# Kernel optimization log

Measured on AMD Instinct MI355X. Metric: run time of the kernel, lower is better.

Reference implementation:

```python
import math
import jax, jax.numpy as jnp
import numpy as np

B, T, C = 2, 768, 64
N_HEAD = 64
HEAD_DIM = C // N_HEAD  # = 1 (forced by the Kronecker-lift shape constraint)


def _alibi_slopes(n_heads):
    def pow2_slopes(n):
        start = 2 ** (-2 ** (-(math.log2(n) - 3)))
        return [start * (start ** i) for i in range(n)]
    if math.log2(n_heads).is_integer():
        s = pow2_slopes(n_heads)
    else:
        closest = 2 ** math.floor(math.log2(n_heads))
        s = pow2_slopes(closest)
        s.extend(pow2_slopes(2 * closest)[0::2][: n_heads - closest])
    return np.asarray(s, dtype=np.float32)


def _kron_block_apply(z, tmp):
    """Apply M.T where M = block_diag_h(kron(eye(hd), tmp[h])). z:(B,T,C), tmp:(H,hd,hd).
    Per head-block, for z reshaped (a,d) over (hd,hd): out[a,c] = sum_d tmp[h,c,d] * z[a,d]."""
    Bz, Tz, Cz = z.shape
    H, hd, _ = tmp.shape
    zr = z.reshape(Bz, Tz, H, hd, hd)
    return jnp.einsum('bthad,hcd->bthac', zr, tmp).reshape(Bz, Tz, Cz)


def setup_inputs() -> dict:
    key = jax.random.key(0)
    kx, kw, kv, kp = jax.random.split(key, 4)
    x = jax.random.normal(kx, (B, T, C), dtype=jnp.float32)
    W_attn = jax.random.normal(kw, (2 * C, C), dtype=jnp.float32) * 0.02
    v_tmp = jax.random.normal(kv, (N_HEAD, HEAD_DIM, HEAD_DIM), dtype=jnp.float32)
    proj_tmp = jax.random.normal(kp, (N_HEAD, HEAD_DIM, HEAD_DIM), dtype=jnp.float32)
    return {"x": x, "W_attn": W_attn, "v_tmp": v_tmp, "proj_tmp": proj_tmp}


def reference(x, W_attn, v_tmp, proj_tmp):
    Bx, Tx, Cx = x.shape
    H = v_tmp.shape[0]
    head_dim = Cx // H
    # q, k projection (use_v=True -> c_attn maps C -> 2C, no bias)
    qk = x @ W_attn.T
    q, k = jnp.split(qk, 2, axis=-1)
    # Kronecker-lifted V transform (block-diagonal structure applied directly)
    v = _kron_block_apply(x, v_tmp)
    # (B,T,H,d) -> (B,H,T,d)
    q = q.reshape(Bx, Tx, H, head_dim).transpose(0, 2, 1, 3)
    k = k.reshape(Bx, Tx, H, head_dim).transpose(0, 2, 1, 3)
    v = v.reshape(Bx, Tx, H, head_dim).transpose(0, 2, 1, 3)
    scale = 1.0 / math.sqrt(head_dim)
    scores = jnp.einsum('bhid,bhjd->bhij', q, k) * scale
    # ALiBi bias: positions clamped at 0 (NOTE: source has no causal -inf mask)
    pos = jnp.minimum(jnp.arange(Tx)[None, :] - jnp.arange(Tx)[:, None], 0).astype(x.dtype)
    slopes = jnp.asarray(_alibi_slopes(H), dtype=x.dtype)
    scores = scores + slopes[None, :, None, None] * pos[None, None, :, :]
    w = jax.nn.softmax(scores, axis=-1)
    y = jnp.einsum('bhij,bhjd->bhid', w, v)
    y = y.transpose(0, 2, 1, 3).reshape(Bx, Tx, Cx)
    # Kronecker-lifted output projection
    y = _kron_block_apply(y, proj_tmp)
    return y
```

## Files before the change

### kernel.cpp

```cpp
#include <hip/hip_runtime.h>
#include <stdint.h>

constexpr int Tc = 768;
constexpr int Hc = 64;
constexpr int Bc = 2;
constexpr int NT = 12;
constexpr int NM = 6;
constexpr int MB = 4 * NM;
constexpr float LOG2E = 1.44269504088896f;
constexpr float LN2   = 0.69314718056f;
constexpr size_t SLAB = (size_t)Bc * Hc * Tc;

typedef float v2f __attribute__((ext_vector_type(2)));
typedef float v4f __attribute__((ext_vector_type(4)));

__global__ __launch_bounds__(64) void proj_mom_kernel(
    const float* __restrict__ x, const float* __restrict__ W,
    const float* __restrict__ vtmp, const float* __restrict__ ptmp,
    float* __restrict__ qs, float* __restrict__ ks, float* __restrict__ vs,
    float* __restrict__ MOM)
{
    const int lane = threadIdx.x & 63;
    const int bx   = blockIdx.x;
    const int b    = bx / NT;
    const int B    = bx - b * NT;
    const int t    = B * 64 + lane;
    const int g    = bx * 64 + lane;
    const int h    = blockIdx.y;
    const int bh   = b * Hc + h;

    const v4f* xp = (const v4f*)(x + (size_t)g * 64);
    const float* __restrict__ wq = W + h * 64;
    const float* __restrict__ wk = W + (64 + h) * 64;
    float aq = 0.f, ak = 0.f;
#pragma unroll
    for (int c = 0; c < 16; ++c) {
        v4f u = xp[c];
        aq = fmaf(u.x, wq[4*c],   aq);  ak = fmaf(u.x, wk[4*c],   ak);
        aq = fmaf(u.y, wq[4*c+1], aq);  ak = fmaf(u.y, wk[4*c+1], ak);
        aq = fmaf(u.z, wq[4*c+2], aq);  ak = fmaf(u.z, wk[4*c+2], ak);
        aq = fmaf(u.w, wq[4*c+3], aq);  ak = fmaf(u.w, wk[4*c+3], ak);
    }
    const float vv = x[(size_t)g * 64 + h] * vtmp[h] * ptmp[h];
    const size_t o = (size_t)bh * Tc + t;
    qs[o] = aq * LOG2E;
    ks[o] = ak;
    vs[o] = vv;

    const float slope2 = exp2f(-0.125f * (float)(h + 1)) * LOG2E;
    const float lf = exp2f(slope2 * (float)(lane - 63));

    float km[NM];
    km[0] = 1.f;
#pragma unroll
    for (int m = 1; m < NM; ++m) km[m] = km[m - 1] * ak;

    float r[MB];
#pragma unroll
    for (int m = 0; m < NM; ++m) {
        const float kl2 = km[m] * lf;
        r[m]           = km[m];
        r[NM + m]      = km[m] * vv;
        r[2 * NM + m]  = kl2;
        r[3 * NM + m]  = kl2 * vv;
    }
#define DPP_PASS(CTRL)                                                        \
    _Pragma("unroll")                                                         \
    for (int ii = 0; ii < MB; ++ii)                                           \
        r[ii] += __int_as_float(__builtin_amdgcn_update_dpp(                  \
            0, __float_as_int(r[ii]), CTRL, 0xf, 0xf, true));
    DPP_PASS(0x111)
    DPP_PASS(0x112)
    DPP_PASS(0x114)
    DPP_PASS(0x118)
    DPP_PASS(0x142)
    DPP_PASS(0x143)
#undef DPP_PASS

    if (lane == 63) {
        float* mp = MOM + ((size_t)bh * NT + B) * MB;
#pragma unroll
        for (int m = 0; m < MB / 4; ++m) {
            v4f s4 = { r[4*m], r[4*m+1], r[4*m+2], r[4*m+3] };
            *(v4f*)(mp + 4 * m) = s4;
        }
    }
}

__global__ __launch_bounds__(256, 6) void attn_kernel(
    const float* __restrict__ qs, const float* __restrict__ ks,
    const float* __restrict__ vs, const float* __restrict__ MOM,
    float* __restrict__ out)
{
    const int tid  = threadIdx.x;
    const int lane = tid & 63;
    const int w    = __builtin_amdgcn_readfirstlane(tid >> 6);
    const int rt   = blockIdx.x;
    const int h    = blockIdx.y;
    const int b    = blockIdx.z;
    const int bh   = b * Hc + h;

    __shared__ float momL[NT * MB];
    __shared__ float kd[64], vd[64];
    __shared__ float comb[MB];
    __shared__ float psum[4][64], pacc[4][64];

    {
        const float* __restrict__ mbp = MOM + (size_t)bh * (NT * MB);
        if (tid < 96) {
            momL[tid]       = mbp[tid];
            momL[tid + 96]  = mbp[tid + 96];
            momL[tid + 192] = mbp[tid + 192];
        } else if (tid < 160) {
            kd[tid - 96] = ks[(size_t)bh * Tc + rt * 64 + (tid - 96)];
        } else if (tid < 224) {
            vd[tid - 160] = vs[(size_t)bh * Tc + rt * 64 + (tid - 160)];
        }
    }
    const float slope2 = exp2f(-0.125f * (float)(h + 1)) * LOG2E;
    __syncthreads();

    if (tid < MB) {
        const int grp = tid >= 2 * NM;
        const int m   = tid - (grp ? 2 * NM : 0);
        float acc = 0.f;
        if (!grp) {
            for (int B = rt + 1; B < NT; ++B)
                acc += momL[B * MB + m];
        } else {
            float wgt = exp2f(-slope2);
            const float ratio = exp2f(-64.f * slope2);
            for (int B = rt - 1; B >= 0; --B) {
                acc = fmaf(wgt, momL[B * MB + 2 * NM + m], acc);
                wgt *= ratio;
            }
        }
        comb[tid] = acc;
    }
    __syncthreads();

    const int i = rt * 64 + lane;
    const float q2 = qs[(size_t)bh * Tc + i];
    const float fi2 = slope2 * (float)i;

    const float z  = q2 * LN2;
    const float p1 = z;
    const float p2 = z * p1 * 0.5f;
    const float p3 = z * p2 * (1.f / 3.f);
    const float p4 = z * p3 * 0.25f;
    const float p5 = z * p4 * 0.2f;

    float S = 0.f, A = 0.f;
    if (w == 0) {
        float sf = comb[0];
        sf = fmaf(p1, comb[1], sf); sf = fmaf(p2, comb[2], sf);
        sf = fmaf(p3, comb[3], sf); sf = fmaf(p4, comb[4], sf);
        sf = fmaf(p5, comb[5], sf);
        float af = comb[6];
        af = fmaf(p1, comb[7],  af); af = fmaf(p2, comb[8],  af);
        af = fmaf(p3, comb[9],  af); af = fmaf(p4, comb[10], af);
        af = fmaf(p5, comb[11], af);
        float sp = comb[12];
        sp = fmaf(p1, comb[13], sp); sp = fmaf(p2, comb[14], sp);
        sp = fmaf(p3, comb[15], sp); sp = fmaf(p4, comb[16], sp);
        sp = fmaf(p5, comb[17], sp);
        float ap = comb[18];
        ap = fmaf(p1, comb[19], ap); ap = fmaf(p2, comb[20], ap);
        ap = fmaf(p3, comb[21], ap); ap = fmaf(p4, comb[22], ap);
        ap = fmaf(p5, comb[23], ap);
        const float f = __builtin_amdgcn_exp2f(-slope2 * (float)lane);
        S = fmaf(f, sp, sf);
        A = fmaf(f, ap, af);
    }

    v2f cu2[8];
#pragma unroll
    for (int u = 0; u < 8; ++u) {
        cu2[u].x = slope2 * (float)(2 * u);
        cu2[u].y = slope2 * (float)(2 * u + 1);
    }
    const float mb = slope2 * (float)(rt * 64 + 16 * w) - fi2;
    const v2f mb2 = {mb, mb};
    const v2f q2v = {q2, q2};
    v2f sum2 = {0.f, 0.f}, acc2 = {0.f, 0.f};
    const v2f* __restrict__ k2p = (const v2f*)kd;
    const v2f* __restrict__ v2p = (const v2f*)vd;
#pragma unroll
    for (int u = 0; u < 8; ++u) {
        v2f k2 = k2p[8 * w + u];
        v2f v2 = v2p[8 * w + u];
        v2f t2 = mb2 + cu2[u];
        v2f bias;
        bias.x = fminf(t2.x, 0.f);
        bias.y = fminf(t2.y, 0.f);
        v2f sc = q2v * k2 + bias;
        v2f e;
        e.x = __builtin_amdgcn_exp2f(sc.x);
        e.y = __builtin_amdgcn_exp2f(sc.y);
        sum2 += e;
        acc2 = e * v2 + acc2;
    }
    S += sum2.x + sum2.y;
    A += acc2.x + acc2.y;

    psum[w][lane] = S;
    pacc[w][lane] = A;
    __syncthreads();

    if (tid < 64) {
        float s = psum[0][lane] + psum[1][lane] + psum[2][lane] + psum[3][lane];
        float a = pacc[0][lane] + pacc[1][lane] + pacc[2][lane] + pacc[3][lane];
        out[((size_t)(b * Tc + rt * 64 + lane)) * 64 + h] =
            a * __builtin_amdgcn_rcpf(s);
    }
}

extern "C" void kernel_launch(void* const* d_in, const int* in_sizes, int n_in,
                              void* d_out, int out_size, void* d_ws, size_t ws_size,
                              hipStream_t stream) {
    const float* x    = (const float*)d_in[0];
    const float* W    = (const float*)d_in[1];
    const float* vtmp = (const float*)d_in[2];
    const float* ptmp = (const float*)d_in[3];
    float* out = (float*)d_out;

    float* qsl = (float*)d_ws;
    float* ksl = qsl + SLAB;
    float* vsl = ksl + SLAB;
    float* mom = vsl + SLAB;

    proj_mom_kernel<<<dim3(24, Hc), 64, 0, stream>>>(
        x, W, vtmp, ptmp, qsl, ksl, vsl, mom);
    attn_kernel<<<dim3(NT, Hc, Bc), 256, 0, stream>>>(
        qsl, ksl, vsl, mom, out);
}
```

Measured before the change: 67.84 us.

## Fuse projection, moment computation and attention into one kernel per head-half

Merges the projection/moment kernel and the attention kernel into a single launch with a grid of 2 halves x heads x batch. Each block recomputes q, k and v for all 768 tokens of its head into shared memory, builds the per-tile moments and prefix combinations locally, then has each thread handle one or two query rows across the full 64-key local window. This removes the second kernel launch and the global round trip through workspace, but it duplicates the projection work across the two halves. It also cuts the grid to 256 blocks with serial per-row loops, which reduces parallelism.

```diff
diff --git a/kernel.cpp b/kernel.cpp
--- a/kernel.cpp
+++ b/kernel.cpp
@@ -9,120 +9,96 @@
 constexpr int MB = 4 * NM;
 constexpr float LOG2E = 1.44269504088896f;
 constexpr float LN2   = 0.69314718056f;
-constexpr size_t SLAB = (size_t)Bc * Hc * Tc;
 
 typedef float v2f __attribute__((ext_vector_type(2)));
 typedef float v4f __attribute__((ext_vector_type(4)));
 
-__global__ __launch_bounds__(64) void proj_mom_kernel(
-    const float* __restrict__ x, const float* __restrict__ W,
-    const float* __restrict__ vtmp, const float* __restrict__ ptmp,
-    float* __restrict__ qs, float* __restrict__ ks, float* __restrict__ vs,
-    float* __restrict__ MOM)
-{
-    const int lane = threadIdx.x & 63;
-    const int bx   = blockIdx.x;
-    const int b    = bx / NT;
-    const int B    = bx - b * NT;
-    const int t    = B * 64 + lane;
-    const int g    = bx * 64 + lane;
-    const int h    = blockIdx.y;
-    const int bh   = b * Hc + h;
-
-    const v4f* xp = (const v4f*)(x + (size_t)g * 64);
-    const float* __restrict__ wq = W + h * 64;
-    const float* __restrict__ wk = W + (64 + h) * 64;
-    float aq = 0.f, ak = 0.f;
-#pragma unroll
-    for (int c = 0; c < 16; ++c) {
-        v4f u = xp[c];
-        aq = fmaf(u.x, wq[4*c],   aq);  ak = fmaf(u.x, wk[4*c],   ak);
-        aq = fmaf(u.y, wq[4*c+1], aq);  ak = fmaf(u.y, wk[4*c+1], ak);
-        aq = fmaf(u.z, wq[4*c+2], aq);  ak = fmaf(u.z, wk[4*c+2], ak);
-        aq = fmaf(u.w, wq[4*c+3], aq);  ak = fmaf(u.w, wk[4*c+3], ak);
-    }
-    const float vv = x[(size_t)g * 64 + h] * vtmp[h] * ptmp[h];
-    const size_t o = (size_t)bh * Tc + t;
-    qs[o] = aq * LOG2E;
-    ks[o] = ak;
-    vs[o] = vv;
-
-    const float slope2 = exp2f(-0.125f * (float)(h + 1)) * LOG2E;
-    const float lf = exp2f(slope2 * (float)(lane - 63));
-
-    float km[NM];
-    km[0] = 1.f;
-#pragma unroll
-    for (int m = 1; m < NM; ++m) km[m] = km[m - 1] * ak;
-
-    float r[MB];
-#pragma unroll
-    for (int m = 0; m < NM; ++m) {
-        const float kl2 = km[m] * lf;
-        r[m]           = km[m];
-        r[NM + m]      = km[m] * vv;
-        r[2 * NM + m]  = kl2;
-        r[3 * NM + m]  = kl2 * vv;
-    }
-#define DPP_PASS(CTRL)                                                        \
-    _Pragma("unroll")                                                         \
-    for (int ii = 0; ii < MB; ++ii)                                           \
-        r[ii] += __int_as_float(__builtin_amdgcn_update_dpp(                  \
-            0, __float_as_int(r[ii]), CTRL, 0xf, 0xf, true));
-    DPP_PASS(0x111)
-    DPP_PASS(0x112)
-    DPP_PASS(0x114)
-    DPP_PASS(0x118)
-    DPP_PASS(0x142)
-    DPP_PASS(0x143)
-#undef DPP_PASS
-
-    if (lane == 63) {
-        float* mp = MOM + ((size_t)bh * NT + B) * MB;
-#pragma unroll
-        for (int m = 0; m < MB / 4; ++m) {
-            v4f s4 = { r[4*m], r[4*m+1], r[4*m+2], r[4*m+3] };
-            *(v4f*)(mp + 4 * m) = s4;
-        }
-    }
-}
-
-__global__ __launch_bounds__(256, 6) void attn_kernel(
-    const float* __restrict__ qs, const float* __restrict__ ks,
-    const float* __restrict__ vs, const float* __restrict__ MOM,
+__global__ __launch_bounds__(256) void fused_attn_kernel(
+    const float* __restrict__ x,
+    const float* __restrict__ W,
+    const float* __restrict__ vtmp,
+    const float* __restrict__ ptmp,
     float* __restrict__ out)
 {
     const int tid  = threadIdx.x;
     const int lane = tid & 63;
     const int w    = __builtin_amdgcn_readfirstlane(tid >> 6);
-    const int rt   = blockIdx.x;
+    const int half = blockIdx.x;
     const int h    = blockIdx.y;
     const int b    = blockIdx.z;
-    const int bh   = b * Hc + h;
-
+
+    __shared__ float kl[Tc], vl[Tc], ql[Tc];
     __shared__ float momL[NT * MB];
-    __shared__ float kd[64], vd[64];
-    __shared__ float comb[MB];
-    __shared__ float psum[4][64], pacc[4][64];
-
-    {
-        const float* __restrict__ mbp = MOM + (size_t)bh * (NT * MB);
-        if (tid < 96) {
-            momL[tid]       = mbp[tid];
-            momL[tid + 96]  = mbp[tid + 96];
-            momL[tid + 192] = mbp[tid + 192];
-        } else if (tid < 160) {
-            kd[tid - 96] = ks[(size_t)bh * Tc + rt * 64 + (tid - 96)];
-        } else if (tid < 224) {
-            vd[tid - 160] = vs[(size_t)bh * Tc + rt * 64 + (tid - 160)];
-        }
-    }
+    __shared__ float combL[NT * MB];
+
+    const float* __restrict__ xb = x + (size_t)b * Tc * 64;
+    const float* __restrict__ wq = W + h * 64;
+    const float* __restrict__ wk = W + (64 + h) * 64;
+    const float vp = vtmp[h] * ptmp[h];
     const float slope2 = exp2f(-0.125f * (float)(h + 1)) * LOG2E;
+
+#pragma unroll
+    for (int rr = 0; rr < 3; ++rr) {
+        const int t = tid + 256 * rr;
+        const v4f* xp = (const v4f*)(xb + (size_t)t * 64);
+        float aq = 0.f, ak = 0.f;
+#pragma unroll
+        for (int c = 0; c < 16; ++c) {
+            v4f u = xp[c];
+            aq = fmaf(u.x, wq[4*c],   aq);  ak = fmaf(u.x, wk[4*c],   ak);
+            aq = fmaf(u.y, wq[4*c+1], aq);  ak = fmaf(u.y, wk[4*c+1], ak);
+            aq = fmaf(u.z, wq[4*c+2], aq);  ak = fmaf(u.z, wk[4*c+2], ak);
+            aq = fmaf(u.w, wq[4*c+3], aq);  ak = fmaf(u.w, wk[4*c+3], ak);
+        }
+        kl[t] = ak;
+        ql[t] = aq * LOG2E;
+        vl[t] = xb[(size_t)t * 64 + h] * vp;
+    }
     __syncthreads();
 
-    if (tid < MB) {
-        const int grp = tid >= 2 * NM;
-        const int m   = tid - (grp ? 2 * NM : 0);
+    const float lf = exp2f(slope2 * (float)(lane - 63));
+#pragma unroll
+    for (int bb = 0; bb < 3; ++bb) {
+        const int B = w + 4 * bb;
+        const float kk = kl[B * 64 + lane];
+        const float vv = vl[B * 64 + lane];
+        float km[NM];
+        km[0] = 1.f;
+#pragma unroll
+        for (int m = 1; m < NM; ++m) km[m] = km[m - 1] * kk;
+        float r[MB];
+#pragma unroll
+        for (int m = 0; m < NM; ++m) {
+            const float kl2 = km[m] * lf;
+            r[m]           = km[m];
+            r[NM + m]      = km[m] * vv;
+            r[2 * NM + m]  = kl2;
+            r[3 * NM + m]  = kl2 * vv;
+        }
+#define DPP_PASS(CTRL)                                                        \
+        _Pragma("unroll")                                                     \
+        for (int ii = 0; ii < MB; ++ii)                                       \
+            r[ii] += __int_as_float(__builtin_amdgcn_update_dpp(              \
+                0, __float_as_int(r[ii]), CTRL, 0xf, 0xf, true));
+        DPP_PASS(0x111)
+        DPP_PASS(0x112)
+        DPP_PASS(0x114)
+        DPP_PASS(0x118)
+        DPP_PASS(0x142)
+        DPP_PASS(0x143)
+#undef DPP_PASS
+        if (lane == 63) {
+#pragma unroll
+            for (int m = 0; m < MB; ++m) momL[B * MB + m] = r[m];
+        }
+    }
+    __syncthreads();
+
+    for (int idx = tid; idx < NT * MB; idx += 256) {
+        const int rt = idx / MB;
+        const int mi = idx - rt * MB;
+        const int grp = mi >= 2 * NM;
+        const int m   = mi - (grp ? 2 * NM : 0);
         float acc = 0.f;
         if (!grp) {
             for (int B = rt + 1; B < NT; ++B)
@@ -135,43 +111,9 @@
                 wgt *= ratio;
             }
         }
-        comb[tid] = acc;
+        combL[idx] = acc;
     }
     __syncthreads();
-
-    const int i = rt * 64 + lane;
-    const float q2 = qs[(size_t)bh * Tc + i];
-    const float fi2 = slope2 * (float)i;
-
-    const float z  = q2 * LN2;
-    const float p1 = z;
-    const float p2 = z * p1 * 0.5f;
-    const float p3 = z * p2 * (1.f / 3.f);
-    const float p4 = z * p3 * 0.25f;
-    const float p5 = z * p4 * 0.2f;
-
-    float S = 0.f, A = 0.f;
-    if (w == 0) {
-        float sf = comb[0];
-        sf = fmaf(p1, comb[1], sf); sf = fmaf(p2, comb[2], sf);
-        sf = fmaf(p3, comb[3], sf); sf = fmaf(p4, comb[4], sf);
-        sf = fmaf(p5, comb[5], sf);
-        float af = comb[6];
-        af = fmaf(p1, comb[7],  af); af = fmaf(p2, comb[8],  af);
-        af = fmaf(p3, comb[9],  af); af = fmaf(p4, comb[10], af);
-        af = fmaf(p5, comb[11], af);
-        float sp = comb[12];
-        sp = fmaf(p1, comb[13], sp); sp = fmaf(p2, comb[14], sp);
-        sp = fmaf(p3, comb[15], sp); sp = fmaf(p4, comb[16], sp);
-        sp = fmaf(p5, comb[17], sp);
-        float ap = comb[18];
-        ap = fmaf(p1, comb[19], ap); ap = fmaf(p2, comb[20], ap);
-        ap = fmaf(p3, comb[21], ap); ap = fmaf(p4, comb[22], ap);
-        ap = fmaf(p5, comb[23], ap);
-        const float f = __builtin_amdgcn_exp2f(-slope2 * (float)lane);
-        S = fmaf(f, sp, sf);
-        A = fmaf(f, ap, af);
-    }
 
     v2f cu2[8];
 #pragma unroll
@@ -179,39 +121,71 @@
         cu2[u].x = slope2 * (float)(2 * u);
         cu2[u].y = slope2 * (float)(2 * u + 1);
     }
-    const float mb = slope2 * (float)(rt * 64 + 16 * w) - fi2;
-    const v2f mb2 = {mb, mb};
-    const v2f q2v = {q2, q2};
-    v2f sum2 = {0.f, 0.f}, acc2 = {0.f, 0.f};
-    const v2f* __restrict__ k2p = (const v2f*)kd;
-    const v2f* __restrict__ v2p = (const v2f*)vd;
-#pragma unroll
-    for (int u = 0; u < 8; ++u) {
-        v2f k2 = k2p[8 * w + u];
-        v2f v2 = v2p[8 * w + u];
-        v2f t2 = mb2 + cu2[u];
-        v2f bias;
-        bias.x = fminf(t2.x, 0.f);
-        bias.y = fminf(t2.y, 0.f);
-        v2f sc = q2v * k2 + bias;
-        v2f e;
-        e.x = __builtin_amdgcn_exp2f(sc.x);
-        e.y = __builtin_amdgcn_exp2f(sc.y);
-        sum2 += e;
-        acc2 = e * v2 + acc2;
-    }
-    S += sum2.x + sum2.y;
-    A += acc2.x + acc2.y;
-
-    psum[w][lane] = S;
-    pacc[w][lane] = A;
-    __syncthreads();
-
-    if (tid < 64) {
-        float s = psum[0][lane] + psum[1][lane] + psum[2][lane] + psum[3][lane];
-        float a = pacc[0][lane] + pacc[1][lane] + pacc[2][lane] + pacc[3][lane];
-        out[((size_t)(b * Tc + rt * 64 + lane)) * 64 + h] =
-            a * __builtin_amdgcn_rcpf(s);
+    for (int r0 = 0; r0 < 384; r0 += 256) {
+        const int r = r0 + tid;
+        if (r < 384) {
+            const int i  = half * 384 + r;
+            const int rt = i >> 6;
+            const int il = i & 63;
+            const float q2 = ql[i];
+            const float z  = q2 * LN2;
+            const float p1 = z;
+            const float p2 = z * p1 * 0.5f;
+            const float p3 = z * p2 * (1.f / 3.f);
+            const float p4 = z * p3 * 0.25f;
+            const float p5 = z * p4 * 0.2f;
+
+            const float* __restrict__ cb = &combL[rt * MB];
+            float sf = cb[0];
+            sf = fmaf(p1, cb[1], sf); sf = fmaf(p2, cb[2], sf);
+            sf = fmaf(p3, cb[3], sf); sf = fmaf(p4, cb[4], sf);
+            sf = fmaf(p5, cb[5], sf);
+            float af = cb[6];
+            af = fmaf(p1, cb[7],  af); af = fmaf(p2, cb[8],  af);
+            af = fmaf(p3, cb[9],  af); af = fmaf(p4, cb[10], af);
+            af = fmaf(p5, cb[11], af);
+            float sp = cb[12];
+            sp = fmaf(p1, cb[13], sp); sp = fmaf(p2, cb[14], sp);
+            sp = fmaf(p3, cb[15], sp); sp = fmaf(p4, cb[16], sp);
+            sp = fmaf(p5, cb[17], sp);
+            float ap = cb[18];
+            ap = fmaf(p1, cb[19], ap); ap = fmaf(p2, cb[20], ap);
+            ap = fmaf(p3, cb[21], ap); ap = fmaf(p4, cb[22], ap);
+            ap = fmaf(p5, cb[23], ap);
+            const float f = __builtin_amdgcn_exp2f(-slope2 * (float)il);
+            float S = fmaf(f, sp, sf);
+            float A = fmaf(f, ap, af);
+
+            const float mbd = -slope2 * (float)il;
+            const v2f q2v = {q2, q2};
+            v2f sum2 = {0.f, 0.f}, acc2 = {0.f, 0.f};
+            const v2f* __restrict__ k2p = (const v2f*)&kl[rt * 64];
+            const v2f* __restrict__ v2p = (const v2f*)&vl[rt * 64];
+#pragma unroll
+            for (int cc = 0; cc < 4; ++cc) {
+                const float mbc = mbd + slope2 * (float)(16 * cc);
+                const v2f mb2 = {mbc, mbc};
+#pragma unroll
+                for (int u = 0; u < 8; ++u) {
+                    v2f k2 = k2p[8 * cc + u];
+                    v2f v2 = v2p[8 * cc + u];
+                    v2f t2 = mb2 + cu2[u];
+                    v2f bias;
+                    bias.x = fminf(t2.x, 0.f);
+                    bias.y = fminf(t2.y, 0.f);
+                    v2f sc = q2v * k2 + bias;
+                    v2f e;
+                    e.x = __builtin_amdgcn_exp2f(sc.x);
+                    e.y = __builtin_amdgcn_exp2f(sc.y);
+                    sum2 += e;
+                    acc2 = e * v2 + acc2;
+                }
+            }
+            S += sum2.x + sum2.y;
+            A += acc2.x + acc2.y;
+
+            out[((size_t)(b * Tc + i)) * 64 + h] = A * __builtin_amdgcn_rcpf(S);
+        }
     }
 }
 
@@ -224,13 +198,6 @@
     const float* ptmp = (const float*)d_in[3];
     float* out = (float*)d_out;
 
-    float* qsl = (float*)d_ws;
-    float* ksl = qsl + SLAB;
-    float* vsl = ksl + SLAB;
-    float* mom = vsl + SLAB;
-
-    proj_mom_kernel<<<dim3(24, Hc), 64, 0, stream>>>(
-        x, W, vtmp, ptmp, qsl, ksl, vsl, mom);
-    attn_kernel<<<dim3(NT, Hc, Bc), 256, 0, stream>>>(
-        qsl, ksl, vsl, mom, out);
+    fused_attn_kernel<<<dim3(2, Hc, Bc), 256, 0, stream>>>(
+        x, W, vtmp, ptmp, out);
 }
```

Result: slower. 73.32 us (+8.1%).
